# Kernel optimization log

Hardware: AMD Instinct MI355X
Metric: run time of the kernel (lower is better)

## Reference

```python
import jax, jax.numpy as jnp
import numpy as np
import math

B, L, C, D, H, NLAYERS, DFF = 256, 100, 55, 512, 8, 3, 64


def _pos_embedding(length, d_model):
    pos = np.arange(length, dtype=np.float32)[:, None]
    div = np.exp(np.arange(0, d_model, 2, dtype=np.float32) * (-math.log(10000.0) / d_model))
    pe = np.zeros((length, d_model), dtype=np.float32)
    pe[:, 0::2] = np.sin(pos * div)
    pe[:, 1::2] = np.cos(pos * div)
    return jnp.asarray(pe)


def setup_inputs() -> dict:
    key = jax.random.key(0)
    ks = jax.random.split(key, 12)
    r = lambda k, s, sc: jax.random.normal(k, s, dtype=jnp.float32) * sc
    sD = 1.0 / math.sqrt(D)
    return {
        'x': r(ks[0], (B, L, C), 1.0),
        'tok_w': r(ks[1], (D, C, 3), 1.0 / math.sqrt(3 * C)),  # Conv1d(c_in->d_model, k=3, circular, no bias)
        'pe': _pos_embedding(L, D),
        'Wq': r(ks[2], (NLAYERS, D, D), sD), 'bq': jnp.zeros((NLAYERS, D), jnp.float32),
        'Wk': r(ks[3], (NLAYERS, D, D), sD), 'bk': jnp.zeros((NLAYERS, D), jnp.float32),
        'Wv': r(ks[4], (NLAYERS, D, D), sD), 'bv': jnp.zeros((NLAYERS, D), jnp.float32),
        'Wsig': r(ks[5], (NLAYERS, H, D), sD), 'bsig': jnp.zeros((NLAYERS, H), jnp.float32),
        'Wo': r(ks[6], (NLAYERS, D, D), sD), 'bo': jnp.zeros((NLAYERS, D), jnp.float32),
        'W1': r(ks[7], (NLAYERS, DFF, D), sD), 'b1': jnp.zeros((NLAYERS, DFF), jnp.float32),  # conv1 (1x1)
        'W2': r(ks[8], (NLAYERS, D, DFF), 1.0 / math.sqrt(DFF)), 'b2': jnp.zeros((NLAYERS, D), jnp.float32),  # conv2 (1x1)
        'proj_w': r(ks[9], (C, D), sD), 'proj_b': jnp.zeros((C,), jnp.float32),
    }


def _forward(x, tok_w, pe, Wq, bq, Wk, bk, Wv, bv, Wsig, bsig, Wo, bo, W1, b1, W2, b2, proj_w, proj_b):
    Bx, Lx, _ = x.shape
    nlayers, nH = Wsig.shape[0], Wsig.shape[1]
    d_model = Wq.shape[1]
    dk = d_model // nH
    scale = 1.0 / math.sqrt(dk)
    # token embedding: circular-padded Conv1d(k=3, no bias), then + positional embedding
    xc = jnp.pad(jnp.swapaxes(x, 1, 2), ((0, 0), (0, 0), (1, 1)), mode='wrap')  # [B,C,L+2]
    emb = jax.lax.conv_general_dilated(xc, tok_w, (1,), 'VALID', dimension_numbers=('NCW', 'OIW', 'NCW'))
    h = jnp.swapaxes(emb, 1, 2) + pe[None]  # [B,L,D]
    dist = jnp.abs(jnp.arange(Lx)[:, None] - jnp.arange(Lx)[None, :]).astype(h.dtype)  # |i-j|
    for l in range(nlayers):
        q = h @ Wq[l].T + bq[l]                       # [B,L,D]
        k = (h @ Wk[l].T + bk[l]).reshape(Bx, Lx, nH, dk)
        v = (h @ Wv[l].T + bv[l]).reshape(Bx, Lx, nH, dk)
        # NOTE: source applies sigma projection to the *projected* queries
        sigma = q @ Wsig[l].T + bsig[l]               # [B,L,H]
        qh = q.reshape(Bx, Lx, nH, dk)
        scores = jnp.einsum('blhe,bshe->bhls', qh, k)  # [B,H,L,L]
        series = jax.nn.softmax(scale * scores, axis=-1)
        # Gaussian prior branch (mask_flag=False; computed in source forward,
        # does not feed the module's returned output)
        sg = jnp.swapaxes(sigma, 1, 2)                 # [B,H,L]
        sg = jnp.power(3.0, jax.nn.sigmoid(sg * 5.0) + 1e-5) - 1.0
        sgE = sg[..., None]                            # [B,H,L,1]
        _prior = jnp.exp(-(dist ** 2)[None, None] / (2.0 * sgE ** 2)) / (math.sqrt(2.0 * math.pi) * sgE)
        o = jnp.einsum('bhls,bshd->blhd', series, v).reshape(Bx, Lx, d_model)
        h = h + (o @ Wo[l].T + bo[l])                  # residual 1 (dropout=identity at eval)
        y = jax.nn.gelu(h @ W1[l].T + b1[l], approximate=False)  # conv1 1x1 + gelu
        h = h + (y @ W2[l].T + b2[l])                  # conv2 1x1, residual 2
    return h @ proj_w.T + proj_b                       # [B,L,c_out]


def reference(x, tok_w, pe, Wq, bq, Wk, bk, Wv, bv, Wsig, bsig, Wo, bo, W1, b1, W2, b2, proj_w, proj_b):
    return _forward(x, tok_w, pe, Wq, bq, Wk, bk, Wv, bv, Wsig, bsig, Wo, bo, W1, b1, W2, b2, proj_w, proj_b)
```

## Files before the change

### kernel.cpp

```cpp
#include <hip/hip_runtime.h>
#include <stdint.h>

typedef unsigned short u16;
typedef __attribute__((ext_vector_type(8))) short short8;
typedef __attribute__((ext_vector_type(4))) float f32x4;

#define DEVI __device__ __forceinline__

#define BB   256
#define LL   100
#define CC   55
#define DD   512
#define HH   8
#define DKK  64
#define MM   (BB * LL)
#define KEMB 192
#define NSEG 17

DEVI float bf2f(u16 s) { union { unsigned int u; float f; } x; x.u = ((unsigned int)s) << 16; return x.f; }
DEVI u16 f2bf(float f) {
  union { float f; unsigned int u; } x; x.f = f;
  unsigned int u = x.u;
  return (u16)((u + 0x7FFFu + ((u >> 16) & 1u)) >> 16);
}

DEVI void async_lds16(const u16* gp, u16* lp) {
  __builtin_amdgcn_global_load_lds((const __attribute__((address_space(1))) void*)gp,
                                   (__attribute__((address_space(3))) void*)lp, 16, 0, 0);
}

DEVI void wave_lds_fence() {
  asm volatile("s_waitcnt lgkmcnt(0)" ::: "memory");
  __builtin_amdgcn_wave_barrier();
}

__global__ void detect_dtype(const u16* __restrict__ x, int* __restrict__ flag) {
  __shared__ int cnt[256];
  int tid = threadIdx.x;
  u16 u = x[2 * tid];
  int e = (u >> 7) & 0xFF;
  cnt[tid] = (e >= 0x5F && e <= 0x90) ? 1 : 0;
  __syncthreads();
  for (int s = 128; s > 0; s >>= 1) { if (tid < s) cnt[tid] += cnt[tid + s]; __syncthreads(); }
  if (tid == 0) *flag = (cnt[0] >= 160) ? 0 : 1;
}

struct Segs { const void* src[NSEG]; int off[NSEG + 1]; };

__global__ void convert_all(Segs s, const int* __restrict__ flag, u16* __restrict__ dst) {
  int i = blockIdx.x * 256 + threadIdx.x;
  if (i >= s.off[NSEG]) return;
  int sidx = 0;
#pragma unroll
  for (int k = 1; k < NSEG; k++) if (i >= s.off[k]) sidx = k;
  int j = i - s.off[sidx];
  u16 v;
  if (*flag) v = f2bf(((const float*)s.src[sidx])[j]);
  else       v = ((const u16*)s.src[sidx])[j];
  dst[i] = v;
}

__global__ void repack_w(const u16* __restrict__ tokw, u16* __restrict__ Wg) {
  int idx = blockIdx.x * 256 + threadIdx.x;
  if (idx >= 512 * KEMB) return;
  int d = idx / KEMB, j = idx % KEMB, k = j >> 6, c = j & 63;
  Wg[idx] = (c < CC) ? tokw[d * (CC * 3) + c * 3 + k] : (u16)0;
}

__global__ void repack_x(const u16* __restrict__ x, u16* __restrict__ Xg) {
  int idx = blockIdx.x * 256 + threadIdx.x;
  if (idx >= MM * KEMB) return;
  int m = idx / KEMB, j = idx % KEMB, k = j >> 6, c = j & 63;
  int b = m / LL, l = m % LL;
  int l2 = l + k - 1; l2 = (l2 + LL) % LL;
  Xg[idx] = (c < CC) ? x[(size_t)(b * LL + l2) * CC + c] : (u16)0;
}

struct GemmW { const u16* W[3]; const u16* bias[3]; void* out[3]; };

template<int BM, int BN, int NTT, int TAG, bool QKV, bool DIRECT>
__global__ __launch_bounds__(256)
void gemm_bt(const u16* __restrict__ A, int K, GemmW w,
             const u16* __restrict__ pe,
             const u16* __restrict__ resid,
             int dogelu,
             int ldo, int nvalid,
             const int* __restrict__ dtf)
{
  constexpr int BK = 32;
  constexpr int MI = BM / 32;
  constexpr int CW = BN / 2, NT = CW / 16;
  constexpr int SW = CW + 4;
  constexpr int STAGE_U16 = (BM + BN) * BK * 2;
  __shared__ alignas(16) u16 smem[STAGE_U16];
  u16* As = smem;
  u16* Bs = smem + BM * BK * 2;

  const int tid = threadIdx.x;
  const int lane = tid & 63;
  const int wv = __builtin_amdgcn_readfirstlane(tid >> 6);
  const int wm = wv & 1, wn = wv >> 1;
  const int l15 = lane & 15, qd = lane >> 4;

  const int id = blockIdx.x;
  const int mpx = gridDim.x / (NTT * 8);
  const int xcd = id & 7, slot = id >> 3;
  const int m_t = xcd * mpx + slot / NTT;
  const int n_t = slot % NTT;
  const int m0 = m_t * BM;
  int n0 = n_t * BN;
  int sel = 0, n0l = n0;
  if (QKV) { sel = n0 >> 9; n0l = n0 & 511; }
  const u16* W = w.W[sel];
  const u16* bias = w.bias[sel];
  void* outp = w.out[sel];

  const f32x4 zf = {0.f, 0.f, 0.f, 0.f};
  f32x4 acc[MI][NT];
#pragma unroll
  for (int i = 0; i < MI; i++)
#pragma unroll
    for (int j = 0; j < NT; j++) acc[i][j] = zf;

  for (int k0 = 0; k0 < K; k0 += 2 * BK) {
    __syncthreads();
#pragma unroll
    for (int p = 0; p < 2; p++) {
      u16* Asp = As + p * BM * BK;
      u16* Bsp = Bs + p * BN * BK;
      const int kp = k0 + p * BK;
#pragma unroll
      for (int i = 0; i < BM / 64; i++) {
        int base = i * 256 + wv * 64;
        int idx = base + lane;
        int row = idx >> 2, c8 = (idx & 3) * 8;
        async_lds16(A + (size_t)(m0 + row) * K + kp + c8, Asp + base * 8);
      }
#pragma unroll
      for (int i = 0; i < BN / 64; i++) {
        int base = i * 256 + wv * 64;
        int idx = base + lane;
        int row = idx >> 2, c8 = (idx & 3) * 8;
        int gr = n0l + row; if (gr >= nvalid) gr = nvalid - 1;
        async_lds16(W + (size_t)gr * K + kp + c8, Bsp + base * 8);
      }
    }
    __syncthreads();

#pragma unroll
    for (int p = 0; p < 2; p++) {
      const u16* Asp = As + p * BM * BK;
      const u16* Bsp = Bs + p * BN * BK;
      short8 af[MI], bfr[NT];
#pragma unroll
      for (int mi = 0; mi < MI; mi++)
        af[mi] = *(const short8*)&Asp[(wm * (BM / 2) + mi * 16 + l15) * BK + qd * 8];
#pragma unroll
      for (int ni = 0; ni < NT; ni++)
        bfr[ni] = *(const short8*)&Bsp[(wn * CW + ni * 16 + l15) * BK + qd * 8];
#pragma unroll
      for (int mi = 0; mi < MI; mi++)
#pragma unroll
        for (int ni = 0; ni < NT; ni++)
          acc[mi][ni] = __builtin_amdgcn_mfma_f32_16x16x32_bf16(af[mi], bfr[ni], acc[mi][ni], 0, 0, 0);
    }
  }

  if (DIRECT) {
    const int sf = (dtf != nullptr) ? *dtf : 0;
#pragma unroll
    for (int mi = 0; mi < MI; mi++)
#pragma unroll
      for (int ni = 0; ni < NT; ni++) {
        int gcol = n0l + wn * CW + ni * 16 + l15;
        float bv = (bias && gcol < nvalid) ? bf2f(bias[gcol]) : 0.f;
#pragma unroll
        for (int r = 0; r < 4; r++) {
          int grow = m0 + wm * (BM / 2) + mi * 16 + qd * 4 + r;
          if (gcol < nvalid) {
            float v = acc[mi][ni][r] + bv;
            if (sf) ((float*)outp)[(size_t)grow * ldo + gcol] = v;
            else    ((u16*)outp)[(size_t)grow * ldo + gcol] = f2bf(v);
          }
        }
      }
    return;
  }

  __syncthreads();
  u16* slab = smem + wv * 16 * SW;
#pragma unroll
  for (int mi = 0; mi < MI; mi++) {
    const int lr = wm * (BM / 2) + mi * 16 + qd * 4;
    float v[NT][4];
    if (!QKV && resid) {
#pragma unroll
      for (int ni = 0; ni < NT; ni++) {
        int col = n0l + wn * CW + ni * 16 + l15;
#pragma unroll
        for (int r = 0; r < 4; r++)
          v[ni][r] = bf2f(resid[(size_t)(m0 + lr + r) * DD + col]);
      }
    } else {
#pragma unroll
      for (int ni = 0; ni < NT; ni++)
#pragma unroll
        for (int r = 0; r < 4; r++) v[ni][r] = 0.f;
    }
#pragma unroll
    for (int ni = 0; ni < NT; ni++) {
      const int lc = wn * CW + ni * 16 + l15;
      float bv = bias ? bf2f(bias[n0l + lc]) : 0.f;
#pragma unroll
      for (int r = 0; r < 4; r++) {
        float x = v[ni][r] + acc[mi][ni][r] + bv;
        if (!QKV && pe) x += bf2f(pe[((m0 + lr + r) % LL) * DD + n0l + lc]);
        if (!QKV && dogelu) x = 0.5f * x * (1.f + erff(x * 0.70710678118654752f));
        v[ni][r] = x;
      }
    }
#pragma unroll
    for (int ni = 0; ni < NT; ni++)
#pragma unroll
      for (int r = 0; r < 4; r++)
        slab[(qd * 4 + r) * SW + ni * 16 + l15] = f2bf(v[ni][r]);
    wave_lds_fence();
    if (BN == 128) {
      int r2 = lane >> 2, c2 = (lane & 3) * 16;
      int grow = m0 + wm * (BM / 2) + mi * 16 + r2;
      u16* op = (u16*)outp + (size_t)grow * ldo + n0l + wn * CW + c2;
      *(short8*)&op[0] = *(const short8*)&slab[r2 * SW + c2];
      *(short8*)&op[8] = *(const short8*)&slab[r2 * SW + c2 + 8];
    } else {
      if (lane < 32) {
        int r2 = lane >> 1, c2 = (lane & 1) * 16;
        int grow = m0 + wm * (BM / 2) + mi * 16 + r2;
        u16* op = (u16*)outp + (size_t)grow * ldo + n0l + wn * CW + c2;
        *(short8*)&op[0] = *(const short8*)&slab[r2 * SW + c2];
        *(short8*)&op[8] = *(const short8*)&slab[r2 * SW + c2 + 8];
      }
    }
    wave_lds_fence();
  }
}

__global__ __launch_bounds__(256)
void attn(const u16* __restrict__ qg, const u16* __restrict__ kg,
          const u16* __restrict__ vg, u16* __restrict__ og)
{
  constexpr int LP = 128;
  __shared__ alignas(16) u16 Ks[LP * DKK];
  __shared__ alignas(16) u16 Vt[DKK * LP];
  __shared__ alignas(16) u16 Ps[LP * LP];

  const int bh = blockIdx.x;
  const int b = bh >> 3, h = bh & 7;
  const size_t base = (size_t)b * LL * DD + (size_t)h * DKK;
  const int tid = threadIdx.x, lane = tid & 63, wv = tid >> 6;
  const int l15 = lane & 15, qd = lane >> 4;
  const short8 z8 = {0, 0, 0, 0, 0, 0, 0, 0};

  for (int i = tid; i < LP * 8; i += 256) {
    int row = i >> 3, e8 = (i & 7) * 8;
    short8 val = z8;
    if (row < LL) val = *(const short8*)(kg + base + (size_t)row * DD + e8);
    *(short8*)&Ks[row * DKK + e8] = val;
  }
  for (int i = tid; i < LP * 8; i += 256) {
    int j = i & 127, d0 = (i >> 7) * 8;
    short8 val = z8;
    if (j < LL) val = *(const short8*)(vg + base + (size_t)j * DD + d0);
#pragma unroll
    for (int u = 0; u < 8; u++) Vt[(d0 + u) * LP + j] = (u16)val[u];
  }
  __syncthreads();

  const f32x4 zf = {0.f, 0.f, 0.f, 0.f};
  f32x4 sc[2][8];
#pragma unroll
  for (int it = 0; it < 2; it++)
#pragma unroll
    for (int jt = 0; jt < 8; jt++) sc[it][jt] = zf;

  short8 af[2][2];
#pragma unroll
  for (int it = 0; it < 2; it++) {
    int row = (2 * wv + it) * 16 + l15;
#pragma unroll
    for (int ks = 0; ks < 2; ks++) {
      short8 val = z8;
      if (row < LL) val = *(const short8*)(qg + base + (size_t)row * DD + ks * 32 + qd * 8);
      af[it][ks] = val;
    }
  }
#pragma unroll
  for (int jt = 0; jt < 8; jt++) {
    short8 b0 = *(const short8*)&Ks[(jt * 16 + l15) * DKK + qd * 8];
    short8 b1 = *(const short8*)&Ks[(jt * 16 + l15) * DKK + 32 + qd * 8];
#pragma unroll
    for (int it = 0; it < 2; it++) {
      sc[it][jt] = __builtin_amdgcn_mfma_f32_16x16x32_bf16(af[it][0], b0, sc[it][jt], 0, 0, 0);
      sc[it][jt] = __builtin_amdgcn_mfma_f32_16x16x32_bf16(af[it][1], b1, sc[it][jt], 0, 0, 0);
    }
  }

  constexpr float scale = 0.125f;
#pragma unroll
  for (int it = 0; it < 2; it++) {
    int rb = (2 * wv + it) * 16 + qd * 4;
#pragma unroll
    for (int r = 0; r < 4; r++) {
      float vals[8];
      float mx = -1e30f;
#pragma unroll
      for (int jt = 0; jt < 8; jt++) {
        int col = jt * 16 + l15;
        float vv = sc[it][jt][r] * scale;
        if (col >= LL) vv = -1e30f;
        vals[jt] = vv;
        mx = fmaxf(mx, vv);
      }
#pragma unroll
      for (int off = 1; off < 16; off <<= 1) mx = fmaxf(mx, __shfl_xor(mx, off, 64));
      float s = 0.f;
#pragma unroll
      for (int jt = 0; jt < 8; jt++) { float p = __expf(vals[jt] - mx); vals[jt] = p; s += p; }
#pragma unroll
      for (int off = 1; off < 16; off <<= 1) s += __shfl_xor(s, off, 64);
      float inv = 1.f / s;
      int rowp = rb + r;
#pragma unroll
      for (int jt = 0; jt < 8; jt++) Ps[rowp * LP + jt * 16 + l15] = f2bf(vals[jt] * inv);
    }
  }
  __syncthreads();

  f32x4 oc[2][4];
#pragma unroll
  for (int it = 0; it < 2; it++)
#pragma unroll
    for (int dt = 0; dt < 4; dt++) oc[it][dt] = zf;
#pragma unroll
  for (int ks = 0; ks < 4; ks++) {
    short8 ap[2];
#pragma unroll
    for (int it = 0; it < 2; it++)
      ap[it] = *(const short8*)&Ps[((2 * wv + it) * 16 + l15) * LP + ks * 32 + qd * 8];
#pragma unroll
    for (int dt = 0; dt < 4; dt++) {
      short8 bv = *(const short8*)&Vt[(dt * 16 + l15) * LP + ks * 32 + qd * 8];
#pragma unroll
      for (int it = 0; it < 2; it++)
        oc[it][dt] = __builtin_amdgcn_mfma_f32_16x16x32_bf16(ap[it], bv, oc[it][dt], 0, 0, 0);
    }
  }

  __syncthreads();
  u16* Os = Ps;
#pragma unroll
  for (int it = 0; it < 2; it++) {
    int rb = (2 * wv + it) * 16 + qd * 4;
#pragma unroll
    for (int dt = 0; dt < 4; dt++)
#pragma unroll
      for (int r = 0; r < 4; r++)
        Os[(rb + r) * DKK + dt * 16 + l15] = f2bf(oc[it][dt][r]);
  }
  __syncthreads();
  {
    int row = tid >> 1, c0 = (tid & 1) * 32;
    if (row < LL) {
      u16* op = og + base + (size_t)row * DD + c0;
#pragma unroll
      for (int c = 0; c < 32; c += 8)
        *(short8*)&op[c] = *(const short8*)&Os[row * DKK + c0 + c];
    }
  }
}

extern "C" void kernel_launch(void* const* d_in, const int* in_sizes, int n_in,
                              void* d_out, int out_size, void* d_ws, size_t ws_size,
                              hipStream_t stream)
{
  (void)in_sizes; (void)n_in; (void)out_size; (void)ws_size;

  char* ws = (char*)d_ws;
  size_t off = 0;
  auto alloc = [&](size_t bytes) { char* p = ws + off; off += (bytes + 255) & ~(size_t)255; return p; };
  int* dflag = (int*)alloc(256);
  static const int seg_sizes[NSEG] = {
    MM * CC, DD * CC * 3, LL * DD,
    3 * DD * DD, 3 * DD, 3 * DD * DD, 3 * DD, 3 * DD * DD, 3 * DD,
    3 * DD * DD, 3 * DD, 3 * 64 * DD, 3 * 64, 3 * DD * 64, 3 * DD,
    CC * DD, CC
  };
  static const int seg_input[NSEG] = {0, 1, 2, 3, 4, 5, 6, 7, 8, 11, 12, 13, 14, 15, 16, 17, 18};
  int total = 0, segoff[NSEG + 1];
  for (int i = 0; i < NSEG; i++) { segoff[i] = total; total += seg_sizes[i]; }
  segoff[NSEG] = total;
  u16* canon = (u16*)alloc((size_t)total * 2);

  u16* hbf = (u16*)alloc((size_t)MM * DD * 2);
  u16* qb  = (u16*)alloc((size_t)MM * DD * 2);
  u16* kb  = (u16*)alloc((size_t)MM * DD * 2);
  u16* vb  = (u16*)alloc((size_t)MM * DD * 2);
  u16* ob  = (u16*)alloc((size_t)MM * DD * 2);
  u16* yb  = (u16*)alloc((size_t)MM * 64 * 2);
  u16* Wg  = (u16*)alloc((size_t)512 * KEMB * 2);
  u16* Xg  = qb;

  const u16* xc  = canon + segoff[0];
  const u16* twc = canon + segoff[1];
  const u16* pec = canon + segoff[2];
  const u16* Wqc = canon + segoff[3];  const u16* bqc = canon + segoff[4];
  const u16* Wkc = canon + segoff[5];  const u16* bkc = canon + segoff[6];
  const u16* Wvc = canon + segoff[7];  const u16* bvc = canon + segoff[8];
  const u16* Woc = canon + segoff[9];  const u16* boc = canon + segoff[10];
  const u16* W1c = canon + segoff[11]; const u16* b1c = canon + segoff[12];
  const u16* W2c = canon + segoff[13]; const u16* b2c = canon + segoff[14];
  const u16* pwc = canon + segoff[15]; const u16* pbc = canon + segoff[16];

  Segs sg;
  for (int i = 0; i < NSEG; i++) { sg.src[i] = d_in[seg_input[i]]; sg.off[i] = segoff[i]; }
  sg.off[NSEG] = total;

  dim3 blk(256);
  detect_dtype<<<dim3(1), blk, 0, stream>>>((const u16*)d_in[0], dflag);
  convert_all<<<dim3((total + 255) / 256), blk, 0, stream>>>(sg, dflag, canon);
  repack_w<<<dim3((512 * KEMB + 255) / 256), blk, 0, stream>>>(twc, Wg);
  repack_x<<<dim3((MM * KEMB + 255) / 256), blk, 0, stream>>>(xc, Xg);

  auto W1of = [&](const u16* p) { GemmW g{}; g.W[0] = g.W[1] = g.W[2] = p; return g; };

  { GemmW g = W1of(Wg); g.out[0] = hbf;
    gemm_bt<128, 64, 8, 0, false, false><<<dim3(1600), blk, 0, stream>>>(Xg, KEMB, g, pec, nullptr, 0, DD, DD, nullptr); }

  for (int l = 0; l < 3; l++) {
    const u16* Wq_l = Wqc + (size_t)l * DD * DD; const u16* bq_l = bqc + l * DD;
    const u16* Wk_l = Wkc + (size_t)l * DD * DD; const u16* bk_l = bkc + l * DD;
    const u16* Wv_l = Wvc + (size_t)l * DD * DD; const u16* bv_l = bvc + l * DD;
    const u16* Wo_l = Woc + (size_t)l * DD * DD; const u16* bo_l = boc + l * DD;
    const u16* W1_l = W1c + (size_t)l * 64 * DD; const u16* b1_l = b1c + l * 64;
    const u16* W2_l = W2c + (size_t)l * DD * 64; const u16* b2_l = b2c + l * DD;

    { GemmW g{}; g.W[0] = Wq_l; g.W[1] = Wk_l; g.W[2] = Wv_l;
      g.bias[0] = bq_l; g.bias[1] = bk_l; g.bias[2] = bv_l;
      g.out[0] = qb; g.out[1] = kb; g.out[2] = vb;
      gemm_bt<128, 64, 24, 1, true, false><<<dim3(4800), blk, 0, stream>>>(hbf, DD, g, nullptr, nullptr, 0, DD, DD, nullptr); }

    attn<<<dim3(BB * HH), blk, 0, stream>>>(qb, kb, vb, ob);

    { GemmW g = W1of(Wo_l); g.bias[0] = g.bias[1] = g.bias[2] = bo_l; g.out[0] = g.out[1] = g.out[2] = hbf;
      gemm_bt<128, 64, 8, 2, false, false><<<dim3(1600), blk, 0, stream>>>(ob, DD, g, nullptr, hbf, 0, DD, DD, nullptr); }
    { GemmW g = W1of(W1_l); g.bias[0] = b1_l; g.out[0] = yb;
      gemm_bt<64, 64, 1, 3, false, false><<<dim3(400), blk, 0, stream>>>(hbf, DD, g, nullptr, nullptr, 1, 64, 64, nullptr); }
    { GemmW g = W1of(W2_l); g.bias[0] = g.bias[1] = g.bias[2] = b2_l; g.out[0] = g.out[1] = g.out[2] = hbf;
      gemm_bt<128, 64, 8, 4, false, false><<<dim3(1600), blk, 0, stream>>>(yb, 64, g, nullptr, hbf, 0, DD, DD, nullptr); }
  }
  { GemmW g = W1of(pwc); g.bias[0] = pbc; g.out[0] = d_out;
    gemm_bt<64, 64, 1, 5, false, true><<<dim3(400), blk, 0, stream>>>(hbf, DD, g, nullptr, nullptr, 0, CC, CC, dflag); }
}
```

Baseline: 672.1 us.

## Fuse FFN conv1+GELU+conv2 into one kernel keeping intermediate in LDS

Replaces the two separate FFN GEMM launches (h@W1 with GELU writing a global intermediate, then y@W2 with residual) with a single kernel. Each block computes a 64-row tile of the GELU activation into LDS, then streams W2 in double-buffered chunks to produce all 512 output columns with bias and residual. This removes the global round trip of the 64-wide intermediate and one launch per layer. In exchange, the second GEMM now runs on only 400 blocks, each looping over 8 column chunks, so there is less parallelism than the previous 1600-block launch. The kernel also reads and writes hbf in place, which relies on each block reading only its own rows.

```diff
diff --git a/kernel.cpp b/kernel.cpp
--- a/kernel.cpp
+++ b/kernel.cpp
@@ -245,6 +245,142 @@
 }
 
 __global__ __launch_bounds__(256)
+void ffn_fused(const u16* __restrict__ h, const u16* __restrict__ W1,
+               const u16* __restrict__ b1, const u16* __restrict__ W2,
+               const u16* __restrict__ b2, u16* __restrict__ hout)
+{
+  constexpr int BM = 64, BK = 32, SW = 36;
+  __shared__ alignas(16) u16 smem[4096 + 10496];
+  u16* y      = smem;
+  u16* shared = smem + 4096;
+  u16* As  = shared;
+  u16* Bs  = shared + 4096;
+  u16* Bs2 = shared;
+  u16* slabs = shared + 8192;
+
+  const int tid = threadIdx.x;
+  const int lane = tid & 63;
+  const int wv = __builtin_amdgcn_readfirstlane(tid >> 6);
+  const int wm = wv & 1, wn = wv >> 1;
+  const int l15 = lane & 15, qd = lane >> 4;
+  const int id = blockIdx.x;
+  const int mpx = gridDim.x >> 3;
+  const int m0 = ((id & 7) * mpx + (id >> 3)) * BM;
+
+  const int srow = tid >> 2, sc8 = (tid & 3) * 8;
+  const f32x4 zf = {0.f, 0.f, 0.f, 0.f};
+
+  f32x4 acc[2][2];
+#pragma unroll
+  for (int i = 0; i < 2; i++)
+#pragma unroll
+    for (int j = 0; j < 2; j++) acc[i][j] = zf;
+
+  for (int k0 = 0; k0 < DD; k0 += 64) {
+    __syncthreads();
+#pragma unroll
+    for (int p = 0; p < 2; p++) {
+      const int kp = k0 + p * BK;
+      async_lds16(h  + (size_t)(m0 + srow) * DD + kp + sc8, As + p * 2048 + tid * 8);
+      async_lds16(W1 + (size_t)srow * DD + kp + sc8,        Bs + p * 2048 + tid * 8);
+    }
+    __syncthreads();
+#pragma unroll
+    for (int p = 0; p < 2; p++) {
+      short8 af[2], bfr[2];
+#pragma unroll
+      for (int mi = 0; mi < 2; mi++)
+        af[mi] = *(const short8*)&As[p * 2048 + (wm * 32 + mi * 16 + l15) * BK + qd * 8];
+#pragma unroll
+      for (int ni = 0; ni < 2; ni++)
+        bfr[ni] = *(const short8*)&Bs[p * 2048 + (wn * 32 + ni * 16 + l15) * BK + qd * 8];
+#pragma unroll
+      for (int mi = 0; mi < 2; mi++)
+#pragma unroll
+        for (int ni = 0; ni < 2; ni++)
+          acc[mi][ni] = __builtin_amdgcn_mfma_f32_16x16x32_bf16(af[mi], bfr[ni], acc[mi][ni], 0, 0, 0);
+    }
+  }
+#pragma unroll
+  for (int mi = 0; mi < 2; mi++)
+#pragma unroll
+    for (int ni = 0; ni < 2; ni++) {
+      float bv = bf2f(b1[wn * 32 + ni * 16 + l15]);
+#pragma unroll
+      for (int r = 0; r < 4; r++) {
+        int row = wm * 32 + mi * 16 + qd * 4 + r;
+        float x = acc[mi][ni][r] + bv;
+        x = 0.5f * x * (1.f + erff(x * 0.70710678118654752f));
+        y[wn * 2048 + row * BK + ni * 16 + l15] = f2bf(x);
+      }
+    }
+  __syncthreads();
+
+  auto stage2 = [&](int buf, int nc) {
+#pragma unroll
+    for (int p = 0; p < 2; p++)
+      async_lds16(W2 + (size_t)(nc * 64 + srow) * 64 + p * BK + sc8,
+                  Bs2 + buf * 4096 + p * 2048 + tid * 8);
+  };
+  stage2(0, 0);
+  int cur = 0;
+  u16* slab = slabs + wv * 16 * SW;
+  for (int nc = 0; nc < 8; nc++) {
+    __syncthreads();
+    if (nc + 1 < 8) stage2(cur ^ 1, nc + 1);
+    f32x4 a2[2][2];
+#pragma unroll
+    for (int i = 0; i < 2; i++)
+#pragma unroll
+      for (int j = 0; j < 2; j++) a2[i][j] = zf;
+#pragma unroll
+    for (int p = 0; p < 2; p++) {
+      short8 af[2], bfr[2];
+#pragma unroll
+      for (int mi = 0; mi < 2; mi++)
+        af[mi] = *(const short8*)&y[p * 2048 + (wm * 32 + mi * 16 + l15) * BK + qd * 8];
+#pragma unroll
+      for (int ni = 0; ni < 2; ni++)
+        bfr[ni] = *(const short8*)&Bs2[cur * 4096 + p * 2048 + (wn * 32 + ni * 16 + l15) * BK + qd * 8];
+#pragma unroll
+      for (int mi = 0; mi < 2; mi++)
+#pragma unroll
+        for (int ni = 0; ni < 2; ni++)
+          a2[mi][ni] = __builtin_amdgcn_mfma_f32_16x16x32_bf16(af[mi], bfr[ni], a2[mi][ni], 0, 0, 0);
+    }
+    const int n0l = nc * 64;
+#pragma unroll
+    for (int mi = 0; mi < 2; mi++) {
+      const int lr = wm * 32 + mi * 16 + qd * 4;
+      float v[2][4];
+#pragma unroll
+      for (int ni = 0; ni < 2; ni++) {
+        int col = n0l + wn * 32 + ni * 16 + l15;
+        float bv = bf2f(b2[col]);
+#pragma unroll
+        for (int r = 0; r < 4; r++)
+          v[ni][r] = bf2f(h[(size_t)(m0 + lr + r) * DD + col]) + a2[mi][ni][r] + bv;
+      }
+#pragma unroll
+      for (int ni = 0; ni < 2; ni++)
+#pragma unroll
+        for (int r = 0; r < 4; r++)
+          slab[(qd * 4 + r) * SW + ni * 16 + l15] = f2bf(v[ni][r]);
+      wave_lds_fence();
+      if (lane < 32) {
+        int r2 = lane >> 1, c2 = (lane & 1) * 16;
+        int grow = m0 + wm * 32 + mi * 16 + r2;
+        u16* op = hout + (size_t)grow * DD + n0l + wn * 32 + c2;
+        *(short8*)&op[0] = *(const short8*)&slab[r2 * SW + c2];
+        *(short8*)&op[8] = *(const short8*)&slab[r2 * SW + c2 + 8];
+      }
+      wave_lds_fence();
+    }
+    cur ^= 1;
+  }
+}
+
+__global__ __launch_bounds__(256)
 void attn(const u16* __restrict__ qg, const u16* __restrict__ kg,
           const u16* __restrict__ vg, u16* __restrict__ og)
 {
@@ -405,7 +541,6 @@
   u16* kb  = (u16*)alloc((size_t)MM * DD * 2);
   u16* vb  = (u16*)alloc((size_t)MM * DD * 2);
   u16* ob  = (u16*)alloc((size_t)MM * DD * 2);
-  u16* yb  = (u16*)alloc((size_t)MM * 64 * 2);
   u16* Wg  = (u16*)alloc((size_t)512 * KEMB * 2);
   u16* Xg  = qb;
 
@@ -452,10 +587,8 @@
 
     { GemmW g = W1of(Wo_l); g.bias[0] = g.bias[1] = g.bias[2] = bo_l; g.out[0] = g.out[1] = g.out[2] = hbf;
       gemm_bt<128, 64, 8, 2, false, false><<<dim3(1600), blk, 0, stream>>>(ob, DD, g, nullptr, hbf, 0, DD, DD, nullptr); }
-    { GemmW g = W1of(W1_l); g.bias[0] = b1_l; g.out[0] = yb;
-      gemm_bt<64, 64, 1, 3, false, false><<<dim3(400), blk, 0, stream>>>(hbf, DD, g, nullptr, nullptr, 1, 64, 64, nullptr); }
-    { GemmW g = W1of(W2_l); g.bias[0] = g.bias[1] = g.bias[2] = b2_l; g.out[0] = g.out[1] = g.out[2] = hbf;
-      gemm_bt<128, 64, 8, 4, false, false><<<dim3(1600), blk, 0, stream>>>(yb, 64, g, nullptr, hbf, 0, DD, DD, nullptr); }
+
+    ffn_fused<<<dim3(400), blk, 0, stream>>>(hbf, W1_l, b1_l, W2_l, b2_l, hbf);
   }
   { GemmW g = W1of(pwc); g.bias[0] = pbc; g.out[0] = d_out;
     gemm_bt<64, 64, 1, 5, false, true><<<dim3(400), blk, 0, stream>>>(hbf, DD, g, nullptr, nullptr, 0, CC, CC, dflag); }
```

Result: faster. 653.5 us (-2.8%).
